# Performance work log

Hardware: AMD Instinct MI355X
Metric: run time of the kernel (lower is better)

The kernel has to match this reference:

```python
import jax, jax.numpy as jnp
import numpy as np
from jax import lax

NEG = -1e30  # finite stand-in for -inf so logaddexp grads stay finite


def setup_inputs() -> dict:
    key = jax.random.key(0)
    k1, k2, k3, k4, k5 = jax.random.split(key, 5)
    B, T, L, S = 16, 2048, 256, 8
    return {
        "emissions": jax.random.normal(k1, (B, T, S), dtype=jnp.float32),
        "transition": jax.random.normal(k2, (S, S), dtype=jnp.float32),
        "bos": jax.random.normal(k3, (S,), dtype=jnp.float32),
        "eos": jax.random.normal(k4, (S,), dtype=jnp.float32),
        "lengths": jnp.full((B,), T, dtype=jnp.int32),
        "targets": jax.random.randint(k5, (B, L), 0, 4, dtype=jnp.int32),
        "target_lengths": jnp.full((B,), L, dtype=jnp.int32),
    }


def _den_logz(em, lengths, transition, bos, eos):
    # Exact log-semiring forward over the fully-connected 8-state denominator CRF graph
    # (the limit of k2.intersect_dense_pruned(...).get_tot_scores(log_semiring=True)).
    B, T, S = em.shape
    alpha0 = bos[None, :] + em[:, 0, :]  # (B,S)

    def step(alpha, em_t):
        a = jax.nn.logsumexp(alpha[:, :, None] + transition[None, :, :], axis=1) + em_t
        return a, a

    _, alphas = lax.scan(step, alpha0, jnp.swapaxes(em, 0, 1)[1:])  # (T-1,B,S)
    alphas = jnp.concatenate([alpha0[None], alphas], axis=0)  # (T,B,S)
    fin = alphas[lengths - 1, jnp.arange(B)]  # (B,S) alpha at last valid frame
    return jax.nn.logsumexp(fin + eos[None, :], axis=-1)


def _num_logz(em, lengths, targets, target_lengths, transition, bos, eos):
    # Forward over the target-constrained enter/extend lattice: symbol u must be
    # entered (state targets[u]) exactly once, optionally extended (state targets[u]+4),
    # then the path moves monotonically to symbol u+1.
    B, T, S = em.shape
    L = targets.shape[1]
    b_idx = jnp.arange(B)
    es = targets          # enter-state ids, (B,L)
    xs = targets + 4      # extend-state ids, (B,L)

    t_xx = transition[xs, xs]  # extend_u -> extend_u
    t_ex = transition[es, xs]  # enter_u  -> extend_u
    prev_e = jnp.concatenate([es[:, :1], es[:, :-1]], axis=1)
    prev_x = jnp.concatenate([xs[:, :1], xs[:, :-1]], axis=1)
    t_ee = transition[prev_e, es]  # enter_{u-1}  -> enter_u
    t_xe = transition[prev_x, es]  # extend_{u-1} -> enter_u

    a_e0 = jnp.full((B, L), NEG, dtype=em.dtype)
    a_e0 = a_e0.at[:, 0].set(bos[es[:, 0]] + em[b_idx, 0, es[:, 0]])
    a_x0 = jnp.full((B, L), NEG, dtype=em.dtype)

    def shift(a):  # a[:, u-1], NEG at u=0
        return jnp.concatenate([jnp.full((B, 1), NEG, dtype=a.dtype), a[:, :-1]], axis=1)

    def step(carry, em_t):
        a_e, a_x = carry
        em_e = jnp.take_along_axis(em_t, es, axis=1)  # (B,L)
        em_x = jnp.take_along_axis(em_t, xs, axis=1)
        new_e = em_e + jnp.logaddexp(shift(a_e) + t_ee, shift(a_x) + t_xe)
        new_x = em_x + jnp.logaddexp(a_e + t_ex, a_x + t_xx)
        return (new_e, new_x), (new_e, new_x)

    _, (ae, ax) = lax.scan(step, (a_e0, a_x0), jnp.swapaxes(em, 0, 1)[1:])
    ae = jnp.concatenate([a_e0[None], ae], axis=0)  # (T,B,L)
    ax = jnp.concatenate([a_x0[None], ax], axis=0)
    fin_e = ae[lengths - 1, b_idx]  # (B,L)
    fin_x = ax[lengths - 1, b_idx]
    u = target_lengths - 1
    fe = fin_e[b_idx, u] + eos[es[b_idx, u]]
    fx = fin_x[b_idx, u] + eos[xs[b_idx, u]]
    return jnp.logaddexp(fe, fx)  # (B,)


def reference(emissions, transition, bos, eos, lengths, targets, target_lengths):
    em = emissions.astype(jnp.float32)
    logz_den = _den_logz(em, lengths, transition, bos, eos)
    logz_num = _num_logz(em, lengths, targets, target_lengths, transition, bos, eos)
    # all samples valid by construction (lengths > 0, 0 < target_len <= length)
    return jnp.mean(logz_den - logz_num)
```

## Files before the change

### kernel.cpp

```cpp
#include <hip/hip_runtime.h>
#include <math.h>


#define LOG2E 1.4426950408889634f
#define LN2   0.69314718055994531f
#define CTL_WSHL1  0x130
#define CTL_WSHR1  0x138
#define CTL_ROR(r) (0x120 + (r))

#define AST(p, v) __hip_atomic_store((p), (v), __ATOMIC_RELAXED, __HIP_MEMORY_SCOPE_AGENT)
#define ALD(p)    __hip_atomic_load((p), __ATOMIC_RELAXED, __HIP_MEMORY_SCOPE_AGENT)

template <int CTRL>
__device__ __forceinline__ float fdpp(float x) {
    return __int_as_float(__builtin_amdgcn_update_dpp(
        0, __float_as_int(x), CTRL, 0xF, 0xF, true));
}
template <int CTRL>
__device__ __forceinline__ int idpp(int x) {
    return __builtin_amdgcn_update_dpp(0, x, CTRL, 0xF, 0xF, true);
}

__device__ __forceinline__ void pin() {
#if __has_builtin(__builtin_amdgcn_sched_barrier)
    __builtin_amdgcn_sched_barrier(0);
#else
    asm volatile("" ::: "memory");
#endif
}

__device__ __forceinline__ float fexp2(float x) {
#if __has_builtin(__builtin_amdgcn_exp2f)
    return __builtin_amdgcn_exp2f(x);
#else
    return exp2f(x);
#endif
}
__device__ __forceinline__ float flog2(float x) {
#if __has_builtin(__builtin_amdgcn_logf)
    return __builtin_amdgcn_logf(x);
#else
    return __log2f(x);
#endif
}
__device__ __forceinline__ float lse2(float a, float b) {
    float m = fmaxf(a, b);
    float d = fminf(a, b) - m;
    return m + flog2(1.0f + fexp2(d));
}

struct NumC { float tee[4], txe[4], tex[4], txx[4]; };

__device__ __forceinline__ void numf_step(const float2* p, float* E, float* X,
                                          float teeF, float txeF, const NumC& c) {
    float nbE = fdpp<CTL_WSHR1>(E[3]);
    float nbX = fdpp<CTL_WSHR1>(X[3]);
    float nE0 = p[0].x * fmaf(nbE,  teeF,     nbX  * txeF);
    float nE1 = p[1].x * fmaf(E[0], c.tee[1], X[0] * c.txe[1]);
    float nE2 = p[2].x * fmaf(E[1], c.tee[2], X[1] * c.txe[2]);
    float nE3 = p[3].x * fmaf(E[2], c.tee[3], X[2] * c.txe[3]);
    float nX0 = p[0].y * fmaf(E[0], c.tex[0], X[0] * c.txx[0]);
    float nX1 = p[1].y * fmaf(E[1], c.tex[1], X[1] * c.txx[1]);
    float nX2 = p[2].y * fmaf(E[2], c.tex[2], X[2] * c.txx[2]);
    float nX3 = p[3].y * fmaf(E[3], c.tex[3], X[3] * c.txx[3]);
    E[0] = nE0; E[1] = nE1; E[2] = nE2; E[3] = nE3;
    X[0] = nX0; X[1] = nX1; X[2] = nX2; X[3] = nX3;
}

__device__ __forceinline__ void numf_boundary(float* E, float* X, int& s,
                                              float& teeF, float& txeF,
                                              int lane, const NumC& c) {
    float m = fmaxf(fmaxf(fmaxf(E[0], E[1]), fmaxf(E[2], E[3])),
                    fmaxf(fmaxf(X[0], X[1]), fmaxf(X[2], X[3])));
    const bool live = (m > 0.0f);
    const int ex = live ? ((int)(__float_as_uint(m) >> 23) - 126) : 0;
    s += ex;
    const int bs = idpp<CTL_WSHR1>(s);
    if (!live) s = bs;
    int d = (lane == 0) ? 0 : (bs - s);
    const int extra = (d > 30) ? d : 0;
    s += extra; d -= extra;
    const float fsc = ldexpf(1.0f, -(ex + extra));
#pragma unroll
    for (int k = 0; k < 4; ++k) { E[k] *= fsc; X[k] *= fsc; }
    const float fs0 = (lane == 0) ? 0.0f : ldexpf(1.0f, d);
    teeF = c.tee[0] * fs0;
    txeF = c.txe[0] * fs0;
}

__device__ __forceinline__ void numb_step(const float2* p, float* bE, float* bX,
                                          const float* tex, const float* txx,
                                          const float* teeN, const float* txeN,
                                          float teeN3F, float txeN3F) {
    float mm0 = p[0].x * bE[0];
    float mm1 = p[1].x * bE[1];
    float mm2 = p[2].x * bE[2];
    float mm3 = p[3].x * bE[3];
    float m10 = p[0].y * bX[0];
    float m11 = p[1].y * bX[1];
    float m12 = p[2].y * bX[2];
    float m13 = p[3].y * bX[3];
    float mup = fdpp<CTL_WSHL1>(mm0);
    float nE0 = fmaf(tex[0], m10, teeN[0] * mm1);
    float nE1 = fmaf(tex[1], m11, teeN[1] * mm2);
    float nE2 = fmaf(tex[2], m12, teeN[2] * mm3);
    float nE3 = fmaf(tex[3], m13, teeN3F   * mup);
    float nX0 = fmaf(txx[0], m10, txeN[0] * mm1);
    float nX1 = fmaf(txx[1], m11, txeN[1] * mm2);
    float nX2 = fmaf(txx[2], m12, txeN[2] * mm3);
    float nX3 = fmaf(txx[3], m13, txeN3F   * mup);
    bE[0] = nE0; bE[1] = nE1; bE[2] = nE2; bE[3] = nE3;
    bX[0] = nX0; bX[1] = nX1; bX[2] = nX2; bX[3] = nX3;
}

__device__ __forceinline__ void numb_boundary(float* bE, float* bX, int& s,
                                              float& teeN3F, float& txeN3F,
                                              int lane, float teeN3, float txeN3) {
    float m = fmaxf(fmaxf(fmaxf(bE[0], bE[1]), fmaxf(bE[2], bE[3])),
                    fmaxf(fmaxf(bX[0], bX[1]), fmaxf(bX[2], bX[3])));
    const bool live = (m > 0.0f);
    const int ex = live ? ((int)(__float_as_uint(m) >> 23) - 126) : 0;
    s += ex;
    const int bs = idpp<CTL_WSHL1>(s);
    if (!live) s = bs;
    int d = (lane == 63) ? 0 : (bs - s);
    const int extra = (d > 30) ? d : 0;
    s += extra; d -= extra;
    const float fsc = ldexpf(1.0f, -(ex + extra));
#pragma unroll
    for (int k = 0; k < 4; ++k) { bE[k] *= fsc; bX[k] *= fsc; }
    const float fs = (lane == 63) ? 0.0f : ldexpf(1.0f, d);
    teeN3F = teeN3 * fs;
    txeN3F = txeN3 * fs;
}

__device__ __forceinline__ void steps4_fwd(const float4 buf[4][2], float* E, float* X,
                                           float teeF, float txeF, const NumC& c) {
#pragma unroll
    for (int q = 0; q < 4; ++q) {
        float2 p[4];
#pragma unroll
        for (int k = 0; k < 4; ++k) {
            const float4 v = buf[k][q >> 1];
            p[k] = (q & 1) ? make_float2(v.z, v.w) : make_float2(v.x, v.y);
        }
        numf_step(p, E, X, teeF, txeF, c);
    }
}
__device__ __forceinline__ void steps4_bwd(const float4 buf[4][2], float* bE, float* bX,
                                           const float* tex, const float* txx,
                                           const float* teeN, const float* txeN,
                                           float teeN3F, float txeN3F) {
#pragma unroll
    for (int q = 0; q < 4; ++q) {
        const int h = 1 - (q >> 1);
        float2 p[4];
#pragma unroll
        for (int k = 0; k < 4; ++k) {
            const float4 v = buf[k][h];
            p[k] = (q & 1) ? make_float2(v.x, v.y) : make_float2(v.z, v.w);
        }
        numb_step(p, bE, bX, tex, txx, teeN, txeN, teeN3F, txeN3F);
    }
}

__device__ __forceinline__ float denf_step(float al, float emt, const float* Tr) {
    float v1 = fdpp<CTL_ROR(1)>(al);
    float v2 = fdpp<CTL_ROR(2)>(al);
    float v3 = fdpp<CTL_ROR(3)>(al);
    float v4 = fdpp<CTL_ROR(4)>(al);
    float v5 = fdpp<CTL_ROR(5)>(al);
    float v6 = fdpp<CTL_ROR(6)>(al);
    float v7 = fdpp<CTL_ROR(7)>(al);
    float q0 = fmaf(v1, Tr[1], al * Tr[0]);
    float q1 = fmaf(v3, Tr[3], v2 * Tr[2]);
    float q2 = fmaf(v5, Tr[5], v4 * Tr[4]);
    float q3 = fmaf(v7, Tr[7], v6 * Tr[6]);
    return ((q0 + q1) + (q2 + q3)) * emt;
}
__device__ __forceinline__ float denb_step(float al, float emt, const float* TrB) {
    float g  = al * emt;
    float v1 = fdpp<CTL_ROR(7)>(g);
    float v2 = fdpp<CTL_ROR(6)>(g);
    float v3 = fdpp<CTL_ROR(5)>(g);
    float v4 = fdpp<CTL_ROR(4)>(g);
    float v5 = fdpp<CTL_ROR(3)>(g);
    float v6 = fdpp<CTL_ROR(2)>(g);
    float v7 = fdpp<CTL_ROR(1)>(g);
    float q0 = fmaf(v1, TrB[1], g * TrB[0]);
    float q1 = fmaf(v3, TrB[3], v2 * TrB[2]);
    float q2 = fmaf(v5, TrB[5], v4 * TrB[4]);
    float q3 = fmaf(v7, TrB[7], v6 * TrB[6]);
    return (q0 + q1) + (q2 + q3);
}
__device__ __forceinline__ int den_renorm(float& al) {
    float mm = fmaxf(al, fdpp<CTL_ROR(4)>(al));
    mm = fmaxf(mm, fdpp<CTL_ROR(2)>(mm));
    mm = fmaxf(mm, fdpp<CTL_ROR(1)>(mm));
    const int ex = (int)(__float_as_uint(mm) >> 23) - 126;
    al = ldexpf(al, -ex);
    return ex;
}

extern "C" __global__ void __launch_bounds__(128)
crf_fused(const float* __restrict__ em, const float* __restrict__ trans,
          const float* __restrict__ bos, const float* __restrict__ eos,
          const int* __restrict__ lengths, const int* __restrict__ targets,
          const int* __restrict__ tlens,
          float* __restrict__ ws, float* __restrict__ out,
          int B, int T, int S, int L)
{
    extern __shared__ float sm[];
    const int bid  = blockIdx.x;
    const int tid  = threadIdx.x;
    const int lane = tid & 63;
    const int wv   = tid >> 6;
    const int half = S >> 1;
    const int role = bid / B;
    const int b    = bid % B;
    const float* gem = em + (size_t)b * T * S;
    const int len = lengths[b];
    const int tm  = (len - 1) >> 1;
    const int P2  = T + 2;
    const int Th2 = P2 >> 1;

    float* NF  = ws + 16 + (size_t)b * 576;
    float* NB  = ws + 16 + (size_t)B * 576 + (size_t)b * 576;
    float* DEN = ws + 16 + (size_t)(2 * B) * 576;
    int* ticket = (int*)ws;

    if (role < 2) {
        float2* s2 = (float2*)sm;
        for (int t = tid; t < T; t += 128) {
            const float4* gr = (const float4*)(gem + t * S);
            float4 a = gr[0], c4 = gr[1];
            s2[0 * P2 + t] = make_float2(fexp2(a.x * LOG2E), fexp2(c4.x * LOG2E));
            s2[1 * P2 + t] = make_float2(fexp2(a.y * LOG2E), fexp2(c4.y * LOG2E));
            s2[2 * P2 + t] = make_float2(fexp2(a.z * LOG2E), fexp2(c4.z * LOG2E));
            s2[3 * P2 + t] = make_float2(fexp2(a.w * LOG2E), fexp2(c4.w * LOG2E));
        }
    } else {
        for (int t = tid; t < T; t += 128) {
            const float4* gr = (const float4*)(gem + t * S);
            float4 a = gr[0], c4 = gr[1];
            float4 w0, w1;
            w0.x = fexp2(a.x * LOG2E); w0.y = fexp2(c4.x * LOG2E);
            w0.z = fexp2(a.y * LOG2E); w0.w = fexp2(c4.y * LOG2E);
            w1.x = fexp2(a.z * LOG2E); w1.y = fexp2(c4.z * LOG2E);
            w1.z = fexp2(a.w * LOG2E); w1.w = fexp2(c4.w * LOG2E);
            ((float4*)sm)[t * 2]     = w0;
            ((float4*)sm)[t * 2 + 1] = w1;
        }
    }
    __syncthreads();

    if (role == 0 && wv == 0) {
        const float2* s2 = (const float2*)sm;
        const float4* s4 = (const float4*)sm;
        const int u0 = lane * 4;
        int e[4], ep[4];
        const int base = b * L;
#pragma unroll
        for (int k = 0; k < 4; ++k) {
            int u = u0 + k;
            e[k] = targets[base + ((u < L) ? u : (L - 1))];
        }
        ep[0] = (u0 > 0) ? targets[base + u0 - 1] : e[0];
        ep[1] = e[0]; ep[2] = e[1]; ep[3] = e[2];
        NumC c;
#pragma unroll
        for (int k = 0; k < 4; ++k) {
            c.tee[k] = fexp2(trans[ep[k] * S + e[k]] * LOG2E);
            c.txe[k] = fexp2(trans[(ep[k] + half) * S + e[k]] * LOG2E);
            c.tex[k] = fexp2(trans[e[k] * S + e[k] + half] * LOG2E);
            c.txx[k] = fexp2(trans[(e[k] + half) * S + e[k] + half] * LOG2E);
        }
        float E[4] = {0.f,0.f,0.f,0.f}, X[4] = {0.f,0.f,0.f,0.f};
        int s = 0;
        if (lane == 0) E[0] = fexp2(bos[e[0]] * LOG2E) * s2[e[0] * P2].x;
        float teeF = (lane == 0) ? 0.0f : c.tee[0];
        float txeF = (lane == 0) ? 0.0f : c.txe[0];

        int t0 = 1;
        while (t0 <= tm && (t0 & 1)) {
            float2 p[4];
#pragma unroll
            for (int k = 0; k < 4; ++k) p[k] = s2[e[k] * P2 + t0];
            numf_step(p, E, X, teeF, txeF, c);
            ++t0;
        }
        if (t0 + 7 <= tm) {
            float4 A[4][2], Bf[4][2];
#pragma unroll
            for (int k = 0; k < 4; ++k) {
                A[k][0] = s4[e[k] * Th2 + (t0 >> 1)];
                A[k][1] = s4[e[k] * Th2 + ((t0 + 2) >> 1)];
            }
            pin();
            while (t0 + 7 <= tm) {
#pragma unroll
                for (int k = 0; k < 4; ++k) {
                    Bf[k][0] = s4[e[k] * Th2 + ((t0 + 4) >> 1)];
                    Bf[k][1] = s4[e[k] * Th2 + ((t0 + 6) >> 1)];
                }
                pin();
                steps4_fwd(A, E, X, teeF, txeF, c);
#pragma unroll
                for (int k = 0; k < 4; ++k) {
                    A[k][0] = s4[e[k] * Th2 + ((t0 + 8) >> 1)];
                    A[k][1] = s4[e[k] * Th2 + ((t0 + 10) >> 1)];
                }
                pin();
                steps4_fwd(Bf, E, X, teeF, txeF, c);
                numf_boundary(E, X, s, teeF, txeF, lane, c);
                t0 += 8;
            }
        }
        while (t0 <= tm) {
            float2 p[4];
#pragma unroll
            for (int k = 0; k < 4; ++k) p[k] = s2[e[k] * P2 + t0];
            numf_step(p, E, X, teeF, txeF, c);
            ++t0;
        }
#pragma unroll
        for (int k = 0; k < 4; ++k) {
            AST(&NF[lane * 8 + k],     E[k]);
            AST(&NF[lane * 8 + 4 + k], X[k]);
        }
        AST(&NF[512 + lane], __int_as_float(s));
    } else if (role == 1 && wv == 0) {
        const float2* s2 = (const float2*)sm;
        const float4* s4 = (const float4*)sm;
        const int u0 = lane * 4;
        int e[5];
        const int base = b * L;
#pragma unroll
        for (int k = 0; k < 5; ++k) {
            int u = u0 + k;
            e[k] = targets[base + ((u < L) ? u : (L - 1))];
        }
        float tex[4], txx[4], teeN[4], txeN[4];
#pragma unroll
        for (int k = 0; k < 4; ++k) {
            tex[k]  = fexp2(trans[e[k] * S + e[k] + half] * LOG2E);
            txx[k]  = fexp2(trans[(e[k] + half) * S + e[k] + half] * LOG2E);
            teeN[k] = fexp2(trans[e[k] * S + e[k + 1]] * LOG2E);
            txeN[k] = fexp2(trans[(e[k] + half) * S + e[k + 1]] * LOG2E);
        }
        if (lane == 63) { teeN[3] = 0.0f; txeN[3] = 0.0f; }
        float bE[4] = {0.f,0.f,0.f,0.f}, bX[4] = {0.f,0.f,0.f,0.f};
        const int uf = tlens[b] - 1;
        if (lane == (uf >> 2)) {
            const int kf = uf & 3;
            bE[kf] = fexp2(eos[e[kf]] * LOG2E);
            bX[kf] = fexp2(eos[e[kf] + half] * LOG2E);
        }
        int s = 0;
        float teeN3F = teeN[3], txeN3F = txeN[3];

        int t1 = len - 1;
        const int tlo = tm + 1;
        while (t1 >= tlo && !(t1 & 1)) {
            float2 p[4];
#pragma unroll
            for (int k = 0; k < 4; ++k) p[k] = s2[e[k] * P2 + t1];
            numb_step(p, bE, bX, tex, txx, teeN, txeN, teeN3F, txeN3F);
            --t1;
        }
        if (t1 - 7 >= tlo) {
            float4 A[4][2], Bf[4][2];
#pragma unroll
            for (int k = 0; k < 4; ++k) {
                A[k][0] = s4[e[k] * Th2 + ((t1 - 3) >> 1)];
                A[k][1] = s4[e[k] * Th2 + ((t1 - 1) >> 1)];
            }
            pin();
            while (t1 - 7 >= tlo) {
#pragma unroll
                for (int k = 0; k < 4; ++k) {
                    Bf[k][0] = s4[e[k] * Th2 + ((t1 - 7) >> 1)];
                    Bf[k][1] = s4[e[k] * Th2 + ((t1 - 5) >> 1)];
                }
                pin();
                steps4_bwd(A, bE, bX, tex, txx, teeN, txeN, teeN3F, txeN3F);
                const int ta = (t1 - 11 > 0) ? (t1 - 11) : 0;
#pragma unroll
                for (int k = 0; k < 4; ++k) {
                    A[k][0] = s4[e[k] * Th2 + (ta >> 1)];
                    A[k][1] = s4[e[k] * Th2 + ((ta + 2) >> 1)];
                }
                pin();
                steps4_bwd(Bf, bE, bX, tex, txx, teeN, txeN, teeN3F, txeN3F);
                numb_boundary(bE, bX, s, teeN3F, txeN3F, lane, teeN[3], txeN[3]);
                t1 -= 8;
            }
        }
        while (t1 >= tlo) {
            float2 p[4];
#pragma unroll
            for (int k = 0; k < 4; ++k) p[k] = s2[e[k] * P2 + t1];
            numb_step(p, bE, bX, tex, txx, teeN, txeN, teeN3F, txeN3F);
            --t1;
        }
#pragma unroll
        for (int k = 0; k < 4; ++k) {
            AST(&NB[lane * 8 + k],     bE[k]);
            AST(&NB[lane * 8 + 4 + k], bX[k]);
        }
        AST(&NB[512 + lane], __int_as_float(s));
    } else if (role == 2) {
        float* denF  = sm + T * 8 + 16;
        float* denB  = denF + 8;
        int*   denFs = (int*)(denB + 8);
        int*   denBs = denFs + 8;
        const int j  = lane & 7;
        const int jj = ((j & 3) << 1) + (j >> 2);
        if (wv == 0) {
            float Tr[8];
#pragma unroll
            for (int r = 0; r < 8; ++r)
                Tr[r] = fexp2(trans[((j - r) & 7) * S + j] * LOG2E);
            float al = fexp2(bos[j] * LOG2E) * sm[jj];
            int sc = 0;
            int t = 1;
            while (t + 3 <= tm) {
                float c0 = sm[t * 8 + jj];
                float c1 = sm[(t + 1) * 8 + jj];
                float c2 = sm[(t + 2) * 8 + jj];
                float c3 = sm[(t + 3) * 8 + jj];
                pin();
                al = denf_step(al, c0, Tr);
                al = denf_step(al, c1, Tr);
                al = denf_step(al, c2, Tr);
                al = denf_step(al, c3, Tr);
                sc += den_renorm(al);
                t += 4;
            }
            while (t <= tm) { al = denf_step(al, sm[t * 8 + jj], Tr); ++t; }
            if (lane < 8) { denF[j] = al; denFs[j] = sc; }
        } else {
            float TrB[8];
#pragma unroll
            for (int r = 0; r < 8; ++r)
                TrB[r] = fexp2(trans[j * S + ((j + r) & 7)] * LOG2E);
            float al = fexp2(eos[j] * LOG2E);
            int sc = 0;
            int t = len - 1;
            const int tlo = tm + 1;
            while (t - 3 >= tlo) {
                float c0 = sm[t * 8 + jj];
                float c1 = sm[(t - 1) * 8 + jj];
                float c2 = sm[(t - 2) * 8 + jj];
                float c3 = sm[(t - 3) * 8 + jj];
                pin();
                al = denb_step(al, c0, TrB);
                al = denb_step(al, c1, TrB);
                al = denb_step(al, c2, TrB);
                al = denb_step(al, c3, TrB);
                sc += den_renorm(al);
                t -= 4;
            }
            while (t >= tlo) { al = denb_step(al, sm[t * 8 + jj], TrB); --t; }
            if (lane < 8) { denB[j] = al; denBs[j] = sc; }
        }
        __syncthreads();
        if (wv == 0 && lane < 8) {
            const float a  = fmaxf(denF[j], 1e-37f);
            const float bb = fmaxf(denB[j], 1e-37f);
            float part = flog2(a) + flog2(bb) + (float)(denFs[j] + denBs[j]);
            part = lse2(part, __shfl_xor(part, 1, 64));
            part = lse2(part, __shfl_xor(part, 2, 64));
            part = lse2(part, __shfl_xor(part, 4, 64));
            if (j == 0) AST(&DEN[b], part);
        }
    }

    __syncthreads();
    int* wflag = (int*)sm;
    if (tid == 0) {
        __threadfence();
        const int tk = atomicAdd(ticket, 1);
        wflag[0] = (tk == 3 * B - 1) ? 1 : 0;
    }
    __syncthreads();
    if (wflag[0] && tid < 64) {
        __threadfence();
        float acc = 0.0f;
        for (int bb2 = 0; bb2 < B; ++bb2) {
            const float* nf = ws + 16 + (size_t)bb2 * 576;
            const float* nb = ws + 16 + (size_t)B * 576 + (size_t)bb2 * 576;
            float v = 0.0f;
#pragma unroll
            for (int k = 0; k < 8; ++k)
                v = fmaf(ALD(&nf[lane * 8 + k]), ALD(&nb[lane * 8 + k]), v);
            const int st = __float_as_int(ALD(&nf[512 + lane]))
                         + __float_as_int(ALD(&nb[512 + lane]));
            float part = (v > 0.0f) ? (flog2(v) + (float)st) : -3.0e38f;
#pragma unroll
            for (int o = 1; o < 64; o <<= 1)
                part = lse2(part, __shfl_xor(part, o, 64));
            if (lane == 0) acc += ALD(&DEN[bb2]) - part;
        }
        if (lane == 0) out[0] = acc * (LN2 / (float)B);
    }
}

extern "C" void kernel_launch(void* const* d_in, const int* in_sizes, int n_in,
                              void* d_out, int out_size, void* d_ws, size_t ws_size,
                              hipStream_t stream)
{
    const float* em      = (const float*)d_in[0];
    const float* trans   = (const float*)d_in[1];
    const float* bos     = (const float*)d_in[2];
    const float* eos     = (const float*)d_in[3];
    const int*   lengths = (const int*)d_in[4];
    const int*   targets = (const int*)d_in[5];
    const int*   tlens   = (const int*)d_in[6];
    float* out = (float*)d_out;
    float* ws  = (float*)d_ws;

    const int B  = in_sizes[4];
    const int SS = in_sizes[1];
    int S = 1; while (S * S < SS) ++S;
    const int T = in_sizes[0] / (B * S);
    const int L = in_sizes[5] / B;

    const size_t shmem = (size_t)(T * 8 + 80) * sizeof(float);

    (void)hipMemsetAsync(ws, 0, 64, stream);
    hipLaunchKernelGGL(crf_fused, dim3(3 * B), dim3(128), shmem, stream,
                       em, trans, bos, eos, lengths, targets, tlens,
                       ws, out, B, T, S, L);
}
```

Measured before the change: 161.1 us.

## Fuse denominator and numerator recursions into one block per sequence

Result: slower. 184.0 us (+14.2%).

```diff
diff --git a/kernel.cpp b/kernel.cpp
--- a/kernel.cpp
+++ b/kernel.cpp
@@ -211,69 +211,69 @@
           int B, int T, int S, int L)
 {
     extern __shared__ float sm[];
-    const int bid  = blockIdx.x;
+    const int b    = blockIdx.x;
     const int tid  = threadIdx.x;
     const int lane = tid & 63;
     const int wv   = tid >> 6;
     const int half = S >> 1;
-    const int role = bid / B;
-    const int b    = bid % B;
     const float* gem = em + (size_t)b * T * S;
     const int len = lengths[b];
     const int tm  = (len - 1) >> 1;
+    const int tlo = tm + 1;
     const int P2  = T + 2;
     const int Th2 = P2 >> 1;
 
-    float* NF  = ws + 16 + (size_t)b * 576;
-    float* NB  = ws + 16 + (size_t)B * 576 + (size_t)b * 576;
-    float* DEN = ws + 16 + (size_t)(2 * B) * 576;
-    int* ticket = (int*)ws;
-
-    if (role < 2) {
-        float2* s2 = (float2*)sm;
+    float* numFv = sm + 8 * P2;
+    int*   numFs = (int*)(numFv + 512);
+    float* numBv = (float*)(numFs + 64);
+    int*   numBs = (int*)(numBv + 512);
+    float* denFv = (float*)(numBs + 64);
+    int*   denFs = (int*)(denFv + 8);
+    float* res   = (float*)(denFs + 8);
+    int*   wflag = (int*)(res + 2);
+
+    float* wsD   = ws + 16;
+    int*   ticket = (int*)ws;
+
+    {
+        float2* s2w = (float2*)sm;
         for (int t = tid; t < T; t += 128) {
             const float4* gr = (const float4*)(gem + t * S);
             float4 a = gr[0], c4 = gr[1];
-            s2[0 * P2 + t] = make_float2(fexp2(a.x * LOG2E), fexp2(c4.x * LOG2E));
-            s2[1 * P2 + t] = make_float2(fexp2(a.y * LOG2E), fexp2(c4.y * LOG2E));
-            s2[2 * P2 + t] = make_float2(fexp2(a.z * LOG2E), fexp2(c4.z * LOG2E));
-            s2[3 * P2 + t] = make_float2(fexp2(a.w * LOG2E), fexp2(c4.w * LOG2E));
-        }
-    } else {
-        for (int t = tid; t < T; t += 128) {
-            const float4* gr = (const float4*)(gem + t * S);
-            float4 a = gr[0], c4 = gr[1];
-            float4 w0, w1;
-            w0.x = fexp2(a.x * LOG2E); w0.y = fexp2(c4.x * LOG2E);
-            w0.z = fexp2(a.y * LOG2E); w0.w = fexp2(c4.y * LOG2E);
-            w1.x = fexp2(a.z * LOG2E); w1.y = fexp2(c4.z * LOG2E);
-            w1.z = fexp2(a.w * LOG2E); w1.w = fexp2(c4.w * LOG2E);
-            ((float4*)sm)[t * 2]     = w0;
-            ((float4*)sm)[t * 2 + 1] = w1;
+            s2w[0 * P2 + t] = make_float2(fexp2(a.x * LOG2E), fexp2(c4.x * LOG2E));
+            s2w[1 * P2 + t] = make_float2(fexp2(a.y * LOG2E), fexp2(c4.y * LOG2E));
+            s2w[2 * P2 + t] = make_float2(fexp2(a.z * LOG2E), fexp2(c4.z * LOG2E));
+            s2w[3 * P2 + t] = make_float2(fexp2(a.w * LOG2E), fexp2(c4.w * LOG2E));
         }
     }
     __syncthreads();
-
-    if (role == 0 && wv == 0) {
-        const float2* s2 = (const float2*)sm;
-        const float4* s4 = (const float4*)sm;
-        const int u0 = lane * 4;
-        int e[4], ep[4];
-        const int base = b * L;
-#pragma unroll
-        for (int k = 0; k < 4; ++k) {
-            int u = u0 + k;
-            e[k] = targets[base + ((u < L) ? u : (L - 1))];
-        }
-        ep[0] = (u0 > 0) ? targets[base + u0 - 1] : e[0];
-        ep[1] = e[0]; ep[2] = e[1]; ep[3] = e[2];
+    const float2* s2 = (const float2*)sm;
+    const float4* s4 = (const float4*)sm;
+
+    const int u0 = lane * 4;
+    const int base = b * L;
+    int e[5];
+#pragma unroll
+    for (int k = 0; k < 5; ++k) {
+        int u = u0 + k;
+        e[k] = targets[base + ((u < L) ? u : (L - 1))];
+    }
+    const int j = lane & 7;
+    const int djb = (j & 3) * 2 * P2 + (j >> 2);
+#define DEM(t) sm[djb + 2 * (t)]
+
+    if (wv == 0) {
+        int ep0 = (u0 > 0) ? targets[base + u0 - 1] : e[0];
         NumC c;
-#pragma unroll
-        for (int k = 0; k < 4; ++k) {
-            c.tee[k] = fexp2(trans[ep[k] * S + e[k]] * LOG2E);
-            c.txe[k] = fexp2(trans[(ep[k] + half) * S + e[k]] * LOG2E);
-            c.tex[k] = fexp2(trans[e[k] * S + e[k] + half] * LOG2E);
-            c.txx[k] = fexp2(trans[(e[k] + half) * S + e[k] + half] * LOG2E);
+        {
+            int epk[4] = {ep0, e[0], e[1], e[2]};
+#pragma unroll
+            for (int k = 0; k < 4; ++k) {
+                c.tee[k] = fexp2(trans[epk[k] * S + e[k]] * LOG2E);
+                c.txe[k] = fexp2(trans[(epk[k] + half) * S + e[k]] * LOG2E);
+                c.tex[k] = fexp2(trans[e[k] * S + e[k] + half] * LOG2E);
+                c.txx[k] = fexp2(trans[(e[k] + half) * S + e[k] + half] * LOG2E);
+            }
         }
         float E[4] = {0.f,0.f,0.f,0.f}, X[4] = {0.f,0.f,0.f,0.f};
         int s = 0;
@@ -281,21 +281,31 @@
         float teeF = (lane == 0) ? 0.0f : c.tee[0];
         float txeF = (lane == 0) ? 0.0f : c.txe[0];
 
+        float Tr[8];
+#pragma unroll
+        for (int r = 0; r < 8; ++r)
+            Tr[r] = fexp2(trans[((j - r) & 7) * S + j] * LOG2E);
+        float al = fexp2(bos[j] * LOG2E) * DEM(0);
+        int sc = 0;
+
         int t0 = 1;
         while (t0 <= tm && (t0 & 1)) {
             float2 p[4];
 #pragma unroll
             for (int k = 0; k < 4; ++k) p[k] = s2[e[k] * P2 + t0];
             numf_step(p, E, X, teeF, txeF, c);
+            al = denf_step(al, DEM(t0), Tr);
             ++t0;
         }
         if (t0 + 7 <= tm) {
             float4 A[4][2], Bf[4][2];
+            float dc0, dc1, dc2, dc3, dn0, dn1, dn2, dn3;
 #pragma unroll
             for (int k = 0; k < 4; ++k) {
                 A[k][0] = s4[e[k] * Th2 + (t0 >> 1)];
                 A[k][1] = s4[e[k] * Th2 + ((t0 + 2) >> 1)];
             }
+            dc0 = DEM(t0); dc1 = DEM(t0 + 1); dc2 = DEM(t0 + 2); dc3 = DEM(t0 + 3);
             pin();
             while (t0 + 7 <= tm) {
 #pragma unroll
@@ -303,15 +313,32 @@
                     Bf[k][0] = s4[e[k] * Th2 + ((t0 + 4) >> 1)];
                     Bf[k][1] = s4[e[k] * Th2 + ((t0 + 6) >> 1)];
                 }
+                dn0 = DEM(t0 + 4); dn1 = DEM(t0 + 5);
+                dn2 = DEM(t0 + 6); dn3 = DEM(t0 + 7);
                 pin();
                 steps4_fwd(A, E, X, teeF, txeF, c);
-#pragma unroll
-                for (int k = 0; k < 4; ++k) {
-                    A[k][0] = s4[e[k] * Th2 + ((t0 + 8) >> 1)];
-                    A[k][1] = s4[e[k] * Th2 + ((t0 + 10) >> 1)];
+                al = denf_step(al, dc0, Tr);
+                al = denf_step(al, dc1, Tr);
+                al = denf_step(al, dc2, Tr);
+                al = denf_step(al, dc3, Tr);
+                sc += den_renorm(al);
+                {
+                    const int tq = (t0 + 8 + 3 <= tm + 3) ? (t0 + 8) : t0;
+#pragma unroll
+                    for (int k = 0; k < 4; ++k) {
+                        A[k][0] = s4[e[k] * Th2 + (tq >> 1)];
+                        A[k][1] = s4[e[k] * Th2 + ((tq + 2) >> 1)];
+                    }
+                    dc0 = DEM(tq); dc1 = DEM(tq + 1);
+                    dc2 = DEM(tq + 2); dc3 = DEM(tq + 3);
                 }
                 pin();
                 steps4_fwd(Bf, E, X, teeF, txeF, c);
+                al = denf_step(al, dn0, Tr);
+                al = denf_step(al, dn1, Tr);
+                al = denf_step(al, dn2, Tr);
+                al = denf_step(al, dn3, Tr);
+                sc += den_renorm(al);
                 numf_boundary(E, X, s, teeF, txeF, lane, c);
                 t0 += 8;
             }
@@ -321,25 +348,17 @@
 #pragma unroll
             for (int k = 0; k < 4; ++k) p[k] = s2[e[k] * P2 + t0];
             numf_step(p, E, X, teeF, txeF, c);
+            al = denf_step(al, DEM(t0), Tr);
             ++t0;
         }
 #pragma unroll
         for (int k = 0; k < 4; ++k) {
-            AST(&NF[lane * 8 + k],     E[k]);
-            AST(&NF[lane * 8 + 4 + k], X[k]);
-        }
-        AST(&NF[512 + lane], __int_as_float(s));
-    } else if (role == 1 && wv == 0) {
-        const float2* s2 = (const float2*)sm;
-        const float4* s4 = (const float4*)sm;
-        const int u0 = lane * 4;
-        int e[5];
-        const int base = b * L;
-#pragma unroll
-        for (int k = 0; k < 5; ++k) {
-            int u = u0 + k;
-            e[k] = targets[base + ((u < L) ? u : (L - 1))];
-        }
+            numFv[lane * 8 + k]     = E[k];
+            numFv[lane * 8 + 4 + k] = X[k];
+        }
+        numFs[lane] = s;
+        if (lane < 8) { denFv[j] = al; denFs[j] = sc; }
+    } else {
         float tex[4], txx[4], teeN[4], txeN[4];
 #pragma unroll
         for (int k = 0; k < 4; ++k) {
@@ -359,22 +378,31 @@
         int s = 0;
         float teeN3F = teeN[3], txeN3F = txeN[3];
 
+        float TrB[8];
+#pragma unroll
+        for (int r = 0; r < 8; ++r)
+            TrB[r] = fexp2(trans[j * S + ((j + r) & 7)] * LOG2E);
+        float al = fexp2(eos[j] * LOG2E);
+        int sc = 0;
+
         int t1 = len - 1;
-        const int tlo = tm + 1;
         while (t1 >= tlo && !(t1 & 1)) {
             float2 p[4];
 #pragma unroll
             for (int k = 0; k < 4; ++k) p[k] = s2[e[k] * P2 + t1];
             numb_step(p, bE, bX, tex, txx, teeN, txeN, teeN3F, txeN3F);
+            al = denb_step(al, DEM(t1), TrB);
             --t1;
         }
         if (t1 - 7 >= tlo) {
             float4 A[4][2], Bf[4][2];
+            float dc0, dc1, dc2, dc3, dn0, dn1, dn2, dn3;
 #pragma unroll
             for (int k = 0; k < 4; ++k) {
                 A[k][0] = s4[e[k] * Th2 + ((t1 - 3) >> 1)];
                 A[k][1] = s4[e[k] * Th2 + ((t1 - 1) >> 1)];
             }
+            dc0 = DEM(t1); dc1 = DEM(t1 - 1); dc2 = DEM(t1 - 2); dc3 = DEM(t1 - 3);
             pin();
             while (t1 - 7 >= tlo) {
 #pragma unroll
@@ -382,16 +410,32 @@
                     Bf[k][0] = s4[e[k] * Th2 + ((t1 - 7) >> 1)];
                     Bf[k][1] = s4[e[k] * Th2 + ((t1 - 5) >> 1)];
                 }
+                dn0 = DEM(t1 - 4); dn1 = DEM(t1 - 5);
+                dn2 = DEM(t1 - 6); dn3 = DEM(t1 - 7);
                 pin();
                 steps4_bwd(A, bE, bX, tex, txx, teeN, txeN, teeN3F, txeN3F);
-                const int ta = (t1 - 11 > 0) ? (t1 - 11) : 0;
-#pragma unroll
-                for (int k = 0; k < 4; ++k) {
-                    A[k][0] = s4[e[k] * Th2 + (ta >> 1)];
-                    A[k][1] = s4[e[k] * Th2 + ((ta + 2) >> 1)];
+                al = denb_step(al, dc0, TrB);
+                al = denb_step(al, dc1, TrB);
+                al = denb_step(al, dc2, TrB);
+                al = denb_step(al, dc3, TrB);
+                sc += den_renorm(al);
+                {
+                    const int ta = (t1 - 11 > 0) ? (t1 - 11) : 0;
+#pragma unroll
+                    for (int k = 0; k < 4; ++k) {
+                        A[k][0] = s4[e[k] * Th2 + (ta >> 1)];
+                        A[k][1] = s4[e[k] * Th2 + ((ta + 2) >> 1)];
+                    }
+                    dc0 = DEM(ta + 3); dc1 = DEM(ta + 2);
+                    dc2 = DEM(ta + 1); dc3 = DEM(ta);
                 }
                 pin();
                 steps4_bwd(Bf, bE, bX, tex, txx, teeN, txeN, teeN3F, txeN3F);
+                al = denb_step(al, dn0, TrB);
+                al = denb_step(al, dn1, TrB);
+                al = denb_step(al, dn2, TrB);
+                al = denb_step(al, dn3, TrB);
+                sc += den_renorm(al);
                 numb_boundary(bE, bX, s, teeN3F, txeN3F, lane, teeN[3], txeN[3]);
                 t1 -= 8;
             }
@@ -401,109 +445,58 @@
 #pragma unroll
             for (int k = 0; k < 4; ++k) p[k] = s2[e[k] * P2 + t1];
             numb_step(p, bE, bX, tex, txx, teeN, txeN, teeN3F, txeN3F);
+            al = denb_step(al, DEM(t1), TrB);
             --t1;
         }
 #pragma unroll
         for (int k = 0; k < 4; ++k) {
-            AST(&NB[lane * 8 + k],     bE[k]);
-            AST(&NB[lane * 8 + 4 + k], bX[k]);
-        }
-        AST(&NB[512 + lane], __int_as_float(s));
-    } else if (role == 2) {
-        float* denF  = sm + T * 8 + 16;
-        float* denB  = denF + 8;
-        int*   denFs = (int*)(denB + 8);
-        int*   denBs = denFs + 8;
-        const int j  = lane & 7;
-        const int jj = ((j & 3) << 1) + (j >> 2);
-        if (wv == 0) {
-            float Tr[8];
-#pragma unroll
-            for (int r = 0; r < 8; ++r)
-                Tr[r] = fexp2(trans[((j - r) & 7) * S + j] * LOG2E);
-            float al = fexp2(bos[j] * LOG2E) * sm[jj];
-            int sc = 0;
-            int t = 1;
-            while (t + 3 <= tm) {
-                float c0 = sm[t * 8 + jj];
-                float c1 = sm[(t + 1) * 8 + jj];
-                float c2 = sm[(t + 2) * 8 + jj];
-                float c3 = sm[(t + 3) * 8 + jj];
-                pin();
-                al = denf_step(al, c0, Tr);
-                al = denf_step(al, c1, Tr);
-                al = denf_step(al, c2, Tr);
-                al = denf_step(al, c3, Tr);
-                sc += den_renorm(al);
-                t += 4;
+            numBv[lane * 8 + k]     = bE[k];
+            numBv[lane * 8 + 4 + k] = bX[k];
+        }
+        numBs[lane] = s;
+        __syncthreads();
+        {
+            const float a  = fmaxf((lane < 8) ? denFv[j] : 1e-37f, 1e-37f);
+            const float bb = fmaxf(al, 1e-37f);
+            if (lane < 8) {
+                float part = flog2(a) + flog2(bb) + (float)(denFs[j] + sc);
+                part = lse2(part, __shfl_xor(part, 1, 64));
+                part = lse2(part, __shfl_xor(part, 2, 64));
+                part = lse2(part, __shfl_xor(part, 4, 64));
+                if (lane == 0) res[1] = part;
             }
-            while (t <= tm) { al = denf_step(al, sm[t * 8 + jj], Tr); ++t; }
-            if (lane < 8) { denF[j] = al; denFs[j] = sc; }
-        } else {
-            float TrB[8];
-#pragma unroll
-            for (int r = 0; r < 8; ++r)
-                TrB[r] = fexp2(trans[j * S + ((j + r) & 7)] * LOG2E);
-            float al = fexp2(eos[j] * LOG2E);
-            int sc = 0;
-            int t = len - 1;
-            const int tlo = tm + 1;
-            while (t - 3 >= tlo) {
-                float c0 = sm[t * 8 + jj];
-                float c1 = sm[(t - 1) * 8 + jj];
-                float c2 = sm[(t - 2) * 8 + jj];
-                float c3 = sm[(t - 3) * 8 + jj];
-                pin();
-                al = denb_step(al, c0, TrB);
-                al = denb_step(al, c1, TrB);
-                al = denb_step(al, c2, TrB);
-                al = denb_step(al, c3, TrB);
-                sc += den_renorm(al);
-                t -= 4;
-            }
-            while (t >= tlo) { al = denb_step(al, sm[t * 8 + jj], TrB); --t; }
-            if (lane < 8) { denB[j] = al; denBs[j] = sc; }
-        }
-        __syncthreads();
-        if (wv == 0 && lane < 8) {
-            const float a  = fmaxf(denF[j], 1e-37f);
-            const float bb = fmaxf(denB[j], 1e-37f);
-            float part = flog2(a) + flog2(bb) + (float)(denFs[j] + denBs[j]);
-            part = lse2(part, __shfl_xor(part, 1, 64));
-            part = lse2(part, __shfl_xor(part, 2, 64));
-            part = lse2(part, __shfl_xor(part, 4, 64));
-            if (j == 0) AST(&DEN[b], part);
-        }
-    }
-
+        }
+        goto after_sync1;
+    }
     __syncthreads();
-    int* wflag = (int*)sm;
+    {
+        float v = 0.0f;
+#pragma unroll
+        for (int k = 0; k < 8; ++k)
+            v = fmaf(numFv[lane * 8 + k], numBv[lane * 8 + k], v);
+        const int st = numFs[lane] + numBs[lane];
+        float part = (v > 0.0f) ? (flog2(v) + (float)st) : -3.0e38f;
+#pragma unroll
+        for (int o = 1; o < 64; o <<= 1)
+            part = lse2(part, __shfl_xor(part, o, 64));
+        if (lane == 0) res[0] = part;
+    }
+after_sync1:
+    __syncthreads();
     if (tid == 0) {
+        AST(&wsD[b], res[1] - res[0]);
         __threadfence();
         const int tk = atomicAdd(ticket, 1);
-        wflag[0] = (tk == 3 * B - 1) ? 1 : 0;
+        wflag[0] = (tk == (int)gridDim.x - 1) ? 1 : 0;
     }
     __syncthreads();
-    if (wflag[0] && tid < 64) {
+    if (wflag[0] && tid == 0) {
         __threadfence();
         float acc = 0.0f;
-        for (int bb2 = 0; bb2 < B; ++bb2) {
-            const float* nf = ws + 16 + (size_t)bb2 * 576;
-            const float* nb = ws + 16 + (size_t)B * 576 + (size_t)bb2 * 576;
-            float v = 0.0f;
-#pragma unroll
-            for (int k = 0; k < 8; ++k)
-                v = fmaf(ALD(&nf[lane * 8 + k]), ALD(&nb[lane * 8 + k]), v);
-            const int st = __float_as_int(ALD(&nf[512 + lane]))
-                         + __float_as_int(ALD(&nb[512 + lane]));
-            float part = (v > 0.0f) ? (flog2(v) + (float)st) : -3.0e38f;
-#pragma unroll
-            for (int o = 1; o < 64; o <<= 1)
-                part = lse2(part, __shfl_xor(part, o, 64));
-            if (lane == 0) acc += ALD(&DEN[bb2]) - part;
-        }
-        if (lane == 0) out[0] = acc * (LN2 / (float)B);
-    }
+        for (int i = 0; i < B; ++i) acc += ALD(&wsD[i]);
+        out[0] = acc * (LN2 / (float)B);
+    }
+#undef DEM
 }
 
 extern "C" void kernel_launch(void* const* d_in, const int* in_sizes, int n_in,
@@ -526,10 +519,10 @@
     const int T = in_sizes[0] / (B * S);
     const int L = in_sizes[5] / B;
 
-    const size_t shmem = (size_t)(T * 8 + 80) * sizeof(float);
+    const size_t shmem = (size_t)(8 * (T + 2) + 1200) * sizeof(float);
 
     (void)hipMemsetAsync(ws, 0, 64, stream);
-    hipLaunchKernelGGL(crf_fused, dim3(3 * B), dim3(128), shmem, stream,
+    hipLaunchKernelGGL(crf_fused, dim3(B), dim3(128), shmem, stream,
                        em, trans, bos, eos, lengths, targets, tlens,
                        ws, out, B, T, S, L);
 }
```

## Stage exponentiated emissions in global workspace instead of LDS

Applied to the files above, without the earlier changes.

New measurement: 186.5 us. +15.8%, slower.

```diff
diff --git a/kernel.cpp b/kernel.cpp
--- a/kernel.cpp
+++ b/kernel.cpp
@@ -10,6 +10,8 @@
 
 #define AST(p, v) __hip_atomic_store((p), (v), __ATOMIC_RELAXED, __HIP_MEMORY_SCOPE_AGENT)
 #define ALD(p)    __hip_atomic_load((p), __ATOMIC_RELAXED, __HIP_MEMORY_SCOPE_AGENT)
+
+#define STREAM_OFF 32768
 
 template <int CTRL>
 __device__ __forceinline__ float fdpp(float x) {
@@ -210,7 +212,12 @@
           float* __restrict__ ws, float* __restrict__ out,
           int B, int T, int S, int L)
 {
-    extern __shared__ float sm[];
+    __shared__ float denFv[8];
+    __shared__ int   denFs[8];
+    __shared__ float denBv[8];
+    __shared__ int   denBs[8];
+    __shared__ int   wflag[1];
+
     const int bid  = blockIdx.x;
     const int tid  = threadIdx.x;
     const int lane = tid & 63;
@@ -221,6 +228,7 @@
     const float* gem = em + (size_t)b * T * S;
     const int len = lengths[b];
     const int tm  = (len - 1) >> 1;
+    const int tlo = tm + 1;
     const int P2  = T + 2;
     const int Th2 = P2 >> 1;
 
@@ -229,34 +237,24 @@
     float* DEN = ws + 16 + (size_t)(2 * B) * 576;
     int* ticket = (int*)ws;
 
-    if (role < 2) {
-        float2* s2 = (float2*)sm;
+    float* gst = ws + STREAM_OFF + (size_t)bid * 8 * P2;
+
+    {
+        float2* g2 = (float2*)gst;
         for (int t = tid; t < T; t += 128) {
             const float4* gr = (const float4*)(gem + t * S);
             float4 a = gr[0], c4 = gr[1];
-            s2[0 * P2 + t] = make_float2(fexp2(a.x * LOG2E), fexp2(c4.x * LOG2E));
-            s2[1 * P2 + t] = make_float2(fexp2(a.y * LOG2E), fexp2(c4.y * LOG2E));
-            s2[2 * P2 + t] = make_float2(fexp2(a.z * LOG2E), fexp2(c4.z * LOG2E));
-            s2[3 * P2 + t] = make_float2(fexp2(a.w * LOG2E), fexp2(c4.w * LOG2E));
-        }
-    } else {
-        for (int t = tid; t < T; t += 128) {
-            const float4* gr = (const float4*)(gem + t * S);
-            float4 a = gr[0], c4 = gr[1];
-            float4 w0, w1;
-            w0.x = fexp2(a.x * LOG2E); w0.y = fexp2(c4.x * LOG2E);
-            w0.z = fexp2(a.y * LOG2E); w0.w = fexp2(c4.y * LOG2E);
-            w1.x = fexp2(a.z * LOG2E); w1.y = fexp2(c4.z * LOG2E);
-            w1.z = fexp2(a.w * LOG2E); w1.w = fexp2(c4.w * LOG2E);
-            ((float4*)sm)[t * 2]     = w0;
-            ((float4*)sm)[t * 2 + 1] = w1;
+            g2[0 * P2 + t] = make_float2(fexp2(a.x * LOG2E), fexp2(c4.x * LOG2E));
+            g2[1 * P2 + t] = make_float2(fexp2(a.y * LOG2E), fexp2(c4.y * LOG2E));
+            g2[2 * P2 + t] = make_float2(fexp2(a.z * LOG2E), fexp2(c4.z * LOG2E));
+            g2[3 * P2 + t] = make_float2(fexp2(a.w * LOG2E), fexp2(c4.w * LOG2E));
         }
     }
     __syncthreads();
+    const float2* s2 = (const float2*)gst;
+    const float4* s4 = (const float4*)gst;
 
     if (role == 0 && wv == 0) {
-        const float2* s2 = (const float2*)sm;
-        const float4* s4 = (const float4*)sm;
         const int u0 = lane * 4;
         int e[4], ep[4];
         const int base = b * L;
@@ -330,8 +328,6 @@
         }
         AST(&NF[512 + lane], __int_as_float(s));
     } else if (role == 1 && wv == 0) {
-        const float2* s2 = (const float2*)sm;
-        const float4* s4 = (const float4*)sm;
         const int u0 = lane * 4;
         int e[5];
         const int base = b * L;
@@ -360,7 +356,6 @@
         float teeN3F = teeN[3], txeN3F = txeN[3];
 
         int t1 = len - 1;
-        const int tlo = tm + 1;
         while (t1 >= tlo && !(t1 & 1)) {
             float2 p[4];
 #pragma unroll
@@ -410,25 +405,21 @@
         }
         AST(&NB[512 + lane], __int_as_float(s));
     } else if (role == 2) {
-        float* denF  = sm + T * 8 + 16;
-        float* denB  = denF + 8;
-        int*   denFs = (int*)(denB + 8);
-        int*   denBs = denFs + 8;
-        const int j  = lane & 7;
-        const int jj = ((j & 3) << 1) + (j >> 2);
+        const int j = lane & 7;
+        const int djb = (j & 3) * 2 * P2 + (j >> 2);
         if (wv == 0) {
             float Tr[8];
 #pragma unroll
             for (int r = 0; r < 8; ++r)
                 Tr[r] = fexp2(trans[((j - r) & 7) * S + j] * LOG2E);
-            float al = fexp2(bos[j] * LOG2E) * sm[jj];
+            float al = fexp2(bos[j] * LOG2E) * gst[djb];
             int sc = 0;
             int t = 1;
             while (t + 3 <= tm) {
-                float c0 = sm[t * 8 + jj];
-                float c1 = sm[(t + 1) * 8 + jj];
-                float c2 = sm[(t + 2) * 8 + jj];
-                float c3 = sm[(t + 3) * 8 + jj];
+                float c0 = gst[djb + 2 * t];
+                float c1 = gst[djb + 2 * (t + 1)];
+                float c2 = gst[djb + 2 * (t + 2)];
+                float c3 = gst[djb + 2 * (t + 3)];
                 pin();
                 al = denf_step(al, c0, Tr);
                 al = denf_step(al, c1, Tr);
@@ -437,8 +428,8 @@
                 sc += den_renorm(al);
                 t += 4;
             }
-            while (t <= tm) { al = denf_step(al, sm[t * 8 + jj], Tr); ++t; }
-            if (lane < 8) { denF[j] = al; denFs[j] = sc; }
+            while (t <= tm) { al = denf_step(al, gst[djb + 2 * t], Tr); ++t; }
+            if (lane < 8) { denFv[j] = al; denFs[j] = sc; }
         } else {
             float TrB[8];
 #pragma unroll
@@ -447,12 +438,11 @@
             float al = fexp2(eos[j] * LOG2E);
             int sc = 0;
             int t = len - 1;
-            const int tlo = tm + 1;
             while (t - 3 >= tlo) {
-                float c0 = sm[t * 8 + jj];
-                float c1 = sm[(t - 1) * 8 + jj];
-                float c2 = sm[(t - 2) * 8 + jj];
-                float c3 = sm[(t - 3) * 8 + jj];
+                float c0 = gst[djb + 2 * t];
+                float c1 = gst[djb + 2 * (t - 1)];
+                float c2 = gst[djb + 2 * (t - 2)];
+                float c3 = gst[djb + 2 * (t - 3)];
                 pin();
                 al = denb_step(al, c0, TrB);
                 al = denb_step(al, c1, TrB);
@@ -461,13 +451,13 @@
                 sc += den_renorm(al);
                 t -= 4;
             }
-            while (t >= tlo) { al = denb_step(al, sm[t * 8 + jj], TrB); --t; }
-            if (lane < 8) { denB[j] = al; denBs[j] = sc; }
+            while (t >= tlo) { al = denb_step(al, gst[djb + 2 * t], TrB); --t; }
+            if (lane < 8) { denBv[j] = al; denBs[j] = sc; }
         }
         __syncthreads();
         if (wv == 0 && lane < 8) {
-            const float a  = fmaxf(denF[j], 1e-37f);
-            const float bb = fmaxf(denB[j], 1e-37f);
+            const float a  = fmaxf(denFv[j], 1e-37f);
+            const float bb = fmaxf(denBv[j], 1e-37f);
             float part = flog2(a) + flog2(bb) + (float)(denFs[j] + denBs[j]);
             part = lse2(part, __shfl_xor(part, 1, 64));
             part = lse2(part, __shfl_xor(part, 2, 64));
@@ -477,11 +467,10 @@
     }
 
     __syncthreads();
-    int* wflag = (int*)sm;
     if (tid == 0) {
         __threadfence();
         const int tk = atomicAdd(ticket, 1);
-        wflag[0] = (tk == 3 * B - 1) ? 1 : 0;
+        wflag[0] = (tk == (int)gridDim.x - 1) ? 1 : 0;
     }
     __syncthreads();
     if (wflag[0] && tid < 64) {
@@ -526,10 +515,10 @@
     const int T = in_sizes[0] / (B * S);
     const int L = in_sizes[5] / B;
 
-    const size_t shmem = (size_t)(T * 8 + 80) * sizeof(float);
-
+    (void)ws_size;
     (void)hipMemsetAsync(ws, 0, 64, stream);
-    hipLaunchKernelGGL(crf_fused, dim3(3 * B), dim3(128), shmem, stream,
+
+    hipLaunchKernelGGL(crf_fused, dim3(3 * B), dim3(128), 0, stream,
                        em, trans, bos, eos, lengths, targets, tlens,
                        ws, out, B, T, S, L);
 }
```
